# Performance work log

Hardware: AMD Instinct MI355X
Metric: run time of the kernel (lower is better)

The kernel has to match this reference:

```python
import jax, jax.numpy as jnp
import numpy as np


def gcn_conv(x, src, dst, W, b, n_nodes):
    """PyG-style GCNConv: add self-loops, symmetric deg^-1/2 normalization,
    linear transform, scatter-add aggregation to dst, then bias."""
    loop = jnp.arange(n_nodes, dtype=src.dtype)
    s = jnp.concatenate([src, loop])
    d = jnp.concatenate([dst, loop])
    deg = jax.ops.segment_sum(jnp.ones_like(d, x.dtype), d, num_segments=n_nodes)
    dinv = jax.lax.rsqrt(deg)  # deg >= 1 due to self-loops
    norm = dinv[s] * dinv[d]  # [E+N]
    h = x @ W.T  # [N, out]
    msg = h[s] * norm[:, None]  # [E+N, out]
    return jax.ops.segment_sum(msg, d, num_segments=n_nodes) + b


def setup_inputs() -> dict:
    key = jax.random.key(0)
    k = jax.random.split(key, 6)
    N, E, IN, HID, OUT = 100000, 1600000, 128, 128, 64
    x = jax.random.normal(k[0], (N, IN), dtype=jnp.float32)
    edge_index = jax.random.randint(k[1], (2, E), 0, N, dtype=jnp.int64)
    W1 = jax.random.normal(k[2], (HID, IN), dtype=jnp.float32) * 0.05
    b1 = jnp.zeros((HID,), dtype=jnp.float32)
    W2 = jax.random.normal(k[3], (OUT, HID), dtype=jnp.float32) * 0.05
    b2 = jnp.zeros((OUT,), dtype=jnp.float32)
    return {"x": x, "W1": W1, "b1": b1, "W2": W2, "b2": b2, "edge_index": edge_index}


def reference(x, W1, b1, W2, b2, edge_index):
    n_nodes = x.shape[0]
    src, dst = edge_index[0], edge_index[1]
    h = jax.nn.relu(gcn_conv(x, src, dst, W1, b1, n_nodes))
    return gcn_conv(h, src, dst, W2, b2, n_nodes)
```

## Files before the change

kernel.cpp:

```cpp
#include <hip/hip_runtime.h>
#include <hip/hip_bf16.h>


#define IN_F  128
#define HID_F 128
#define OUT_F 64

#define NPB     512
#define MAXBKT  256
#define CHUNK   4096
#define SLAB    12288
#define CAP     12288

typedef __bf16 bf16_t;
typedef __bf16 bf16x4 __attribute__((ext_vector_type(4)));
typedef __bf16 bf16x8 __attribute__((ext_vector_type(8)));
typedef float  f32x2  __attribute__((ext_vector_type(2)));
typedef float  f32x4  __attribute__((ext_vector_type(4)));
typedef unsigned u32x2 __attribute__((ext_vector_type(2)));
typedef unsigned u32x4 __attribute__((ext_vector_type(4)));

__global__ __launch_bounds__(256) void k_part(const int* __restrict__ src,
                                              const int* __restrict__ dst, int E,
                                              int* __restrict__ bcur,
                                              unsigned* __restrict__ part, int NBKT) {
    __shared__ int cnt[MAXBKT];
    __shared__ int base[MAXBKT];
    for (int i = threadIdx.x; i < NBKT; i += 256) cnt[i] = 0;
    __syncthreads();
    int cbase = blockIdx.x * CHUNK;
    int cend = min(cbase + CHUNK, E);
    for (int e = cbase + (int)threadIdx.x; e < cend; e += 256)
        atomicAdd(&cnt[dst[e] >> 9], 1);
    __syncthreads();
    int off = (int)((blockIdx.x * 73u) % (unsigned)NBKT);
    for (int j = threadIdx.x; j < NBKT; j += 256) {
        int i = j + off; if (i >= NBKT) i -= NBKT;
        int c = cnt[i];
        base[i] = c ? (i * SLAB + atomicAdd(&bcur[i * 16], c)) : 0;
        cnt[i] = 0;
    }
    __syncthreads();
    for (int e = cbase + (int)threadIdx.x; e < cend; e += 256) {
        int d = dst[e];
        int b = d >> 9;
        int lp = atomicAdd(&cnt[b], 1);
        part[base[b] + lp] = (unsigned)src[e] | ((unsigned)(d & 511) << 17);
    }
}

__global__ __launch_bounds__(512) void k_bucket(const unsigned* __restrict__ part,
                                                const int* __restrict__ bcur,
                                                int2* __restrict__ off2,
                                                int* __restrict__ col,
                                                float* __restrict__ dinv, int N) {
    __shared__ int lcnt[NPB];
    __shared__ int lexc[NPB];
    __shared__ int lcur[NPB];
    __shared__ int psum[NPB];
    __shared__ int stage[CAP];
    int b = blockIdx.x;
    int t = threadIdx.x;
    int node0 = b * NPB;
    int e0s = b * SLAB;
    int cnt = bcur[b * 16];
    lcnt[t] = 0;
    __syncthreads();
    for (int i = t; i < cnt; i += 512)
        atomicAdd(&lcnt[part[e0s + i] >> 17], 1);
    __syncthreads();
    int pc = (lcnt[t] + 7) & ~7;
    psum[t] = pc;
    __syncthreads();
    for (int ofs = 1; ofs < NPB; ofs <<= 1) {
        int add = (t >= ofs) ? psum[t - ofs] : 0;
        __syncthreads();
        psum[t] += add;
        __syncthreads();
    }
    int run = psum[t] - pc;
    lexc[t] = run;
    lcur[t] = run;
    int node = node0 + t;
    if (node < N) {
        off2[node] = make_int2(e0s + run, e0s + run + pc);
        dinv[node] = rsqrtf((float)lcnt[t] + 1.0f);
    }
    __syncthreads();
    for (int i = t; i < cnt; i += 512) {
        unsigned p = part[e0s + i];
        int dl = p >> 17;
        int sv = (int)(p & 0x1FFFF);
        int lp = atomicAdd(&lcur[dl], 1);
        if (lp < CAP) stage[lp] = sv;
        else col[e0s + lp] = sv;
    }
    __syncthreads();
    {
        int en = lexc[t] + pc;
        for (int i = lcur[t]; i < en; i++) {
            if (i < CAP) stage[i] = N; else col[e0s + i] = N;
        }
    }
    __syncthreads();
    int tot = psum[NPB - 1];
    for (int i = t; i < tot && i < CAP; i += 512) col[e0s + i] = stage[i];
}

template <int NCOL, typename TIN>
__global__ __launch_bounds__(256) void k_gemm_mfma(const TIN* __restrict__ X,
                                                   const float* __restrict__ W,
                                                   const float* __restrict__ scale,
                                                   bf16_t* __restrict__ H, int N) {
    constexpr int CT = NCOL / 16;
    int wv = threadIdx.x >> 6, lane = threadIdx.x & 63;
    int quad = lane >> 4, l16 = lane & 15;
    int row0 = blockIdx.x * 128 + wv * 32;
    f32x4 acc[2][CT] = {};
#pragma unroll
    for (int ks = 0; ks < 4; ks++) {
        int k0 = ks * 32 + quad * 8;
        bf16x8 a[2];
#pragma unroll
        for (int rt = 0; rt < 2; rt++) {
            int r = row0 + rt * 16 + l16;
            if (r >= N) r = N - 1;
            const TIN* p = X + (size_t)r * 128 + k0;
            if constexpr (sizeof(TIN) == 4) {
                f32x4 x0 = *(const f32x4*)p;
                f32x4 x1 = *(const f32x4*)(p + 4);
                bf16x8 tt;
                tt[0] = (bf16_t)x0[0]; tt[1] = (bf16_t)x0[1];
                tt[2] = (bf16_t)x0[2]; tt[3] = (bf16_t)x0[3];
                tt[4] = (bf16_t)x1[0]; tt[5] = (bf16_t)x1[1];
                tt[6] = (bf16_t)x1[2]; tt[7] = (bf16_t)x1[3];
                a[rt] = tt;
            } else {
                a[rt] = *(const bf16x8*)p;
            }
        }
#pragma unroll
        for (int ct = 0; ct < CT; ct++) {
            const float* wp = W + (size_t)(ct * 16 + l16) * 128 + k0;
            f32x4 w0 = *(const f32x4*)wp;
            f32x4 w1 = *(const f32x4*)(wp + 4);
            bf16x8 bfrag;
            bfrag[0] = (bf16_t)w0[0]; bfrag[1] = (bf16_t)w0[1];
            bfrag[2] = (bf16_t)w0[2]; bfrag[3] = (bf16_t)w0[3];
            bfrag[4] = (bf16_t)w1[0]; bfrag[5] = (bf16_t)w1[1];
            bfrag[6] = (bf16_t)w1[2]; bfrag[7] = (bf16_t)w1[3];
#pragma unroll
            for (int rt = 0; rt < 2; rt++)
                acc[rt][ct] = __builtin_amdgcn_mfma_f32_16x16x32_bf16(a[rt], bfrag, acc[rt][ct], 0, 0, 0);
        }
    }
#pragma unroll
    for (int rt = 0; rt < 2; rt++)
#pragma unroll
        for (int r4 = 0; r4 < 4; r4++) {
            int r = row0 + rt * 16 + quad * 4 + r4;
            if (r < N) {
                float sc = scale[r];
#pragma unroll
                for (int ct = 0; ct < CT; ct++)
                    H[(size_t)r * NCOL + ct * 16 + l16] = (bf16_t)(sc * acc[rt][ct][r4]);
            } else if (r == N) {
#pragma unroll
                for (int ct = 0; ct < CT; ct++)
                    H[(size_t)N * NCOL + ct * 16 + l16] = (bf16_t)0.f;
            }
        }
}

template <int ROWE>
__device__ __forceinline__ void gather8(const bf16_t* __restrict__ hp,
                                        const int* __restrict__ col, int e,
                                        u32x4* w) {
    int4 c0 = *(const int4*)(col + e);
    int4 c1 = *(const int4*)(col + e + 4);
    w[0] = *(const u32x4*)(hp + (unsigned)c0.x * (unsigned)ROWE);
    w[1] = *(const u32x4*)(hp + (unsigned)c0.y * (unsigned)ROWE);
    w[2] = *(const u32x4*)(hp + (unsigned)c0.z * (unsigned)ROWE);
    w[3] = *(const u32x4*)(hp + (unsigned)c0.w * (unsigned)ROWE);
    w[4] = *(const u32x4*)(hp + (unsigned)c1.x * (unsigned)ROWE);
    w[5] = *(const u32x4*)(hp + (unsigned)c1.y * (unsigned)ROWE);
    w[6] = *(const u32x4*)(hp + (unsigned)c1.z * (unsigned)ROWE);
    w[7] = *(const u32x4*)(hp + (unsigned)c1.w * (unsigned)ROWE);
}

__device__ __forceinline__ void accum8(const u32x4* w, f32x2* a2) {
#pragma unroll
    for (int u = 0; u < 8; u++)
#pragma unroll
        for (int k = 0; k < 4; k++) {
            f32x2 v;
            v.x = __uint_as_float(w[u][k] << 16);
            v.y = __uint_as_float(w[u][k] & 0xffff0000u);
            a2[k] += v;
        }
}

__global__ __launch_bounds__(256) void k_agg_gemm(const bf16_t* __restrict__ h,
                                                  const int2* __restrict__ off2,
                                                  const int* __restrict__ col,
                                                  const float* __restrict__ dinv,
                                                  const float* __restrict__ bias,
                                                  const float* __restrict__ W2,
                                                  bf16_t* __restrict__ h2, int N) {
    __shared__ float hl[16][132];
    __shared__ float dl[16];
    int lane = threadIdx.x & 63;
    int wv = threadIdx.x >> 6;
    int g = lane >> 4, fl = lane & 15;
    int node0 = blockIdx.x * 16;
    int node = node0 + wv * 4 + g;
    bool alive = node < N;
    int f = fl * 8;
    const bf16_t* hp = h + f;
    f32x2 a2[4] = {};
    float di = 0.f;
    if (alive) {
        u32x4 ws = *(const u32x4*)(hp + (unsigned)node * 128u);
        int2 oe = off2[node];
        di = dinv[node];
#pragma unroll
        for (int k = 0; k < 4; k++) {
            f32x2 v;
            v.x = __uint_as_float(ws[k] << 16);
            v.y = __uint_as_float(ws[k] & 0xffff0000u);
            a2[k] = v;
        }
        u32x4 w[8];
        for (int e = oe.x; e < oe.y; e += 8) {
            gather8<128>(hp, col, e, w);
            accum8(w, a2);
        }
    }
    f32x4 b0 = *(const f32x4*)(bias + f);
    f32x4 b1 = *(const f32x4*)(bias + f + 4);
    int lr = wv * 4 + g;
#pragma unroll
    for (int j = 0; j < 8; j++) {
        float bv = (j < 4) ? b0[j] : b1[j - 4];
        float val = a2[j >> 1][j & 1] * di + bv;
        hl[lr][f + j] = fmaxf(val, 0.f);
    }
    if (fl == 0) dl[lr] = di;
    __syncthreads();

    int quad = lane >> 4, l16 = lane & 15;
    f32x4 c4 = {0.f, 0.f, 0.f, 0.f};
#pragma unroll
    for (int ks = 0; ks < 4; ks++) {
        int k0 = ks * 32 + quad * 8;
        bf16x8 afr;
#pragma unroll
        for (int j = 0; j < 8; j++) afr[j] = (bf16_t)hl[l16][k0 + j];
        const float* wp = W2 + (size_t)(wv * 16 + l16) * 128 + k0;
        f32x4 w0 = *(const f32x4*)wp;
        f32x4 w1 = *(const f32x4*)(wp + 4);
        bf16x8 bfr;
        bfr[0] = (bf16_t)w0[0]; bfr[1] = (bf16_t)w0[1];
        bfr[2] = (bf16_t)w0[2]; bfr[3] = (bf16_t)w0[3];
        bfr[4] = (bf16_t)w1[0]; bfr[5] = (bf16_t)w1[1];
        bfr[6] = (bf16_t)w1[2]; bfr[7] = (bf16_t)w1[3];
        c4 = __builtin_amdgcn_mfma_f32_16x16x32_bf16(afr, bfr, c4, 0, 0, 0);
    }
#pragma unroll
    for (int r4 = 0; r4 < 4; r4++) {
        int rr = quad * 4 + r4;
        int gn = node0 + rr;
        if (gn < N)
            h2[(size_t)gn * 64 + wv * 16 + l16] = (bf16_t)(dl[rr] * c4[r4]);
    }
    if (blockIdx.x == 0 && threadIdx.x < 32)
        ((unsigned*)h2)[(size_t)N * 32 + threadIdx.x] = 0u;
}

template <int ROWE, int LPN, bool RELU, typename TOUT>
__global__ __launch_bounds__(256) void k_agg(const bf16_t* __restrict__ h,
                                             const int2* __restrict__ off2,
                                             const int* __restrict__ col,
                                             const float* __restrict__ dinv,
                                             const float* __restrict__ bias,
                                             TOUT* __restrict__ out, int N) {
    constexpr int NPW = 64 / LPN;
    int lane = threadIdx.x & 63;
    int wv = threadIdx.x >> 6;
    int g = lane / LPN, fl = lane % LPN;
    int node = blockIdx.x * (4 * NPW) + wv * NPW + g;
    if (node >= N) return;
    int f = fl * 8;
    const bf16_t* hp = h + f;
    u32x4 ws = *(const u32x4*)(hp + (unsigned)node * (unsigned)ROWE);
    int2 oe = off2[node];
    float di = dinv[node];
    f32x2 a2[4];
#pragma unroll
    for (int k = 0; k < 4; k++) {
        f32x2 v;
        v.x = __uint_as_float(ws[k] << 16);
        v.y = __uint_as_float(ws[k] & 0xffff0000u);
        a2[k] = v;
    }
    u32x4 w[8];
    for (int e = oe.x; e < oe.y; e += 8) {
        gather8<ROWE>(hp, col, e, w);
        accum8(w, a2);
    }
    f32x4 b0 = *(const f32x4*)(bias + f);
    f32x4 b1 = *(const f32x4*)(bias + f + 4);
    float r[8];
#pragma unroll
    for (int j = 0; j < 8; j++) {
        float bv = (j < 4) ? b0[j] : b1[j - 4];
        float val = a2[j >> 1][j & 1] * di + bv;
        if (RELU) val = fmaxf(val, 0.f);
        r[j] = val;
    }
    if constexpr (sizeof(TOUT) == 2) {
        bf16x8 v;
#pragma unroll
        for (int j = 0; j < 8; j++) v[j] = (bf16_t)r[j];
        *(bf16x8*)((bf16_t*)out + (size_t)node * ROWE + f) = v;
    } else {
        f32x4 v0 = {r[0], r[1], r[2], r[3]};
        f32x4 v1 = {r[4], r[5], r[6], r[7]};
        *(f32x4*)((float*)out + (size_t)node * ROWE + f) = v0;
        *(f32x4*)((float*)out + (size_t)node * ROWE + f + 4) = v1;
    }
}

extern "C" void kernel_launch(void* const* d_in, const int* in_sizes, int n_in,
                              void* d_out, int out_size, void* d_ws, size_t ws_size,
                              hipStream_t stream) {
    const float* x  = (const float*)d_in[0];
    const float* W1 = (const float*)d_in[1];
    const float* b1 = (const float*)d_in[2];
    const float* W2 = (const float*)d_in[3];
    const float* b2 = (const float*)d_in[4];
    const int*   ei = (const int*)d_in[5];

    int N = in_sizes[0] / IN_F;
    int E = in_sizes[5] / 2;
    const int* src = ei;
    const int* dst = ei + E;
    int NBKT = (N + NPB - 1) / NPB;
    int pchunks = (E + CHUNK - 1) / CHUNK;

    size_t woff = 0;
    auto alloc = [&](size_t bytes) {
        void* p = (char*)d_ws + woff;
        woff += (bytes + 255) & ~(size_t)255;
        return p;
    };
    int*      bcur  = (int*)alloc((size_t)NBKT * 16 * 4);
    unsigned* part  = (unsigned*)alloc((size_t)NBKT * SLAB * 4);
    int*      col   = (int*)alloc((size_t)NBKT * SLAB * 4);
    int2*     off2  = (int2*)alloc((size_t)N * 8);
    float*    dinv  = (float*)alloc((size_t)N * 4);
    bf16_t*   h1    = (bf16_t*)alloc((size_t)(N + 1) * HID_F * 2);
    bf16_t*   h2b   = (bf16_t*)alloc((size_t)(N + 1) * OUT_F * 2);
    float*    outp  = (float*)d_out;

    hipMemsetAsync(bcur, 0, (size_t)NBKT * 16 * 4, stream);
    k_part<<<pchunks, 256, 0, stream>>>(src, dst, E, bcur, part, NBKT);
    k_bucket<<<NBKT, 512, 0, stream>>>(part, bcur, off2, col, dinv, N);

    int gemm_blocks = (N + 127) / 128;

    k_gemm_mfma<HID_F, float><<<gemm_blocks, 256, 0, stream>>>(x, W1, dinv, h1, N);
    k_agg_gemm<<<(N + 15) / 16, 256, 0, stream>>>(h1, off2, col, dinv, b1, W2, h2b, N);
    k_agg<OUT_F, 8, false, float><<<(N + 31) / 32, 256, 0, stream>>>(h2b, off2, col, dinv, b2, outp, N);
}
```

Baseline: 271.6 us.

## Stage partition writes in LDS and pre-convert weights to bf16 once

k_part now runs a block-local prefix scan over the bucket counts and stages each edge in shared memory grouped by bucket. It then writes the chunk to the global partition buffer bucket-contiguously, so global stores are coalesced instead of scattered. A new k_pre kernel converts W1 and W2 to bf16 once and also zeroes bcur, replacing the memset. The GEMM kernels then load bf16 weight fragments directly instead of converting fp32 in every block. The staging adds about 24KB of LDS per k_part block and several scan barriers, and the scan assumes NBKT is at most 256.

Result: faster. 251.9 us (-7.3%).

```diff
diff --git a/kernel.cpp b/kernel.cpp
--- a/kernel.cpp
+++ b/kernel.cpp
@@ -20,32 +20,64 @@
 typedef unsigned u32x2 __attribute__((ext_vector_type(2)));
 typedef unsigned u32x4 __attribute__((ext_vector_type(4)));
 
+__global__ __launch_bounds__(256) void k_pre(const float* __restrict__ W1s,
+                                             const float* __restrict__ W2s,
+                                             bf16_t* __restrict__ Wdst,
+                                             int n1, int n2,
+                                             int* __restrict__ bcur, int nb16) {
+    int i = blockIdx.x * 256 + threadIdx.x;
+    if (i < n1) Wdst[i] = (bf16_t)W1s[i];
+    else if (i < n1 + n2) Wdst[i] = (bf16_t)W2s[i - n1];
+    if (blockIdx.x == gridDim.x - 1) {
+        for (int j = threadIdx.x; j < nb16; j += 256) bcur[j] = 0;
+    }
+}
+
 __global__ __launch_bounds__(256) void k_part(const int* __restrict__ src,
                                               const int* __restrict__ dst, int E,
                                               int* __restrict__ bcur,
                                               unsigned* __restrict__ part, int NBKT) {
     __shared__ int cnt[MAXBKT];
     __shared__ int base[MAXBKT];
-    for (int i = threadIdx.x; i < NBKT; i += 256) cnt[i] = 0;
+    __shared__ int cstart[MAXBKT];
+    __shared__ unsigned stg[CHUNK];
+    __shared__ unsigned short sbk[CHUNK];
+    int t = threadIdx.x;
+    cnt[t] = 0;
     __syncthreads();
     int cbase = blockIdx.x * CHUNK;
     int cend = min(cbase + CHUNK, E);
-    for (int e = cbase + (int)threadIdx.x; e < cend; e += 256)
+    int clen = cend - cbase;
+    for (int e = cbase + t; e < cend; e += 256)
         atomicAdd(&cnt[dst[e] >> 9], 1);
     __syncthreads();
-    int off = (int)((blockIdx.x * 73u) % (unsigned)NBKT);
-    for (int j = threadIdx.x; j < NBKT; j += 256) {
-        int i = j + off; if (i >= NBKT) i -= NBKT;
-        int c = cnt[i];
-        base[i] = c ? (i * SLAB + atomicAdd(&bcur[i * 16], c)) : 0;
-        cnt[i] = 0;
-    }
-    __syncthreads();
-    for (int e = cbase + (int)threadIdx.x; e < cend; e += 256) {
+    int c = cnt[t];
+    cstart[t] = c;
+    __syncthreads();
+    for (int ofs = 1; ofs < 256; ofs <<= 1) {
+        int add = (t >= ofs) ? cstart[t - ofs] : 0;
+        __syncthreads();
+        cstart[t] += add;
+        __syncthreads();
+    }
+    int excl = cstart[t] - c;
+    __syncthreads();
+    cstart[t] = excl;
+    base[t] = (c && t < NBKT) ? (t * SLAB + atomicAdd(&bcur[t * 16], c)) : 0;
+    cnt[t] = 0;
+    __syncthreads();
+    for (int e = cbase + t; e < cend; e += 256) {
         int d = dst[e];
         int b = d >> 9;
         int lp = atomicAdd(&cnt[b], 1);
-        part[base[b] + lp] = (unsigned)src[e] | ((unsigned)(d & 511) << 17);
+        int pos = cstart[b] + lp;
+        stg[pos] = (unsigned)src[e] | ((unsigned)(d & 511) << 17);
+        sbk[pos] = (unsigned short)b;
+    }
+    __syncthreads();
+    for (int i = t; i < clen; i += 256) {
+        int b = sbk[i];
+        part[base[b] + (i - cstart[b])] = stg[i];
     }
 }
 
@@ -109,7 +141,7 @@
 
 template <int NCOL, typename TIN>
 __global__ __launch_bounds__(256) void k_gemm_mfma(const TIN* __restrict__ X,
-                                                   const float* __restrict__ W,
+                                                   const bf16_t* __restrict__ W,
                                                    const float* __restrict__ scale,
                                                    bf16_t* __restrict__ H, int N) {
     constexpr int CT = NCOL / 16;
@@ -141,14 +173,7 @@
         }
 #pragma unroll
         for (int ct = 0; ct < CT; ct++) {
-            const float* wp = W + (size_t)(ct * 16 + l16) * 128 + k0;
-            f32x4 w0 = *(const f32x4*)wp;
-            f32x4 w1 = *(const f32x4*)(wp + 4);
-            bf16x8 bfrag;
-            bfrag[0] = (bf16_t)w0[0]; bfrag[1] = (bf16_t)w0[1];
-            bfrag[2] = (bf16_t)w0[2]; bfrag[3] = (bf16_t)w0[3];
-            bfrag[4] = (bf16_t)w1[0]; bfrag[5] = (bf16_t)w1[1];
-            bfrag[6] = (bf16_t)w1[2]; bfrag[7] = (bf16_t)w1[3];
+            bf16x8 bfrag = *(const bf16x8*)(W + (size_t)(ct * 16 + l16) * 128 + k0);
 #pragma unroll
             for (int rt = 0; rt < 2; rt++)
                 acc[rt][ct] = __builtin_amdgcn_mfma_f32_16x16x32_bf16(a[rt], bfrag, acc[rt][ct], 0, 0, 0);
@@ -205,7 +230,7 @@
                                                   const int* __restrict__ col,
                                                   const float* __restrict__ dinv,
                                                   const float* __restrict__ bias,
-                                                  const float* __restrict__ W2,
+                                                  const bf16_t* __restrict__ W2,
                                                   bf16_t* __restrict__ h2, int N) {
     __shared__ float hl[16][132];
     __shared__ float dl[16];
@@ -256,14 +281,7 @@
         bf16x8 afr;
 #pragma unroll
         for (int j = 0; j < 8; j++) afr[j] = (bf16_t)hl[l16][k0 + j];
-        const float* wp = W2 + (size_t)(wv * 16 + l16) * 128 + k0;
-        f32x4 w0 = *(const f32x4*)wp;
-        f32x4 w1 = *(const f32x4*)(wp + 4);
-        bf16x8 bfr;
-        bfr[0] = (bf16_t)w0[0]; bfr[1] = (bf16_t)w0[1];
-        bfr[2] = (bf16_t)w0[2]; bfr[3] = (bf16_t)w0[3];
-        bfr[4] = (bf16_t)w1[0]; bfr[5] = (bf16_t)w1[1];
-        bfr[6] = (bf16_t)w1[2]; bfr[7] = (bf16_t)w1[3];
+        bf16x8 bfr = *(const bf16x8*)(W2 + (size_t)(wv * 16 + l16) * 128 + k0);
         c4 = __builtin_amdgcn_mfma_f32_16x16x32_bf16(afr, bfr, c4, 0, 0, 0);
     }
 #pragma unroll
@@ -359,17 +377,22 @@
     int*      col   = (int*)alloc((size_t)NBKT * SLAB * 4);
     int2*     off2  = (int2*)alloc((size_t)N * 8);
     float*    dinv  = (float*)alloc((size_t)N * 4);
+    bf16_t*   Wb    = (bf16_t*)alloc((size_t)(HID_F * IN_F + OUT_F * HID_F) * 2);
+    bf16_t*   W1b   = Wb;
+    bf16_t*   W2b   = Wb + HID_F * IN_F;
     bf16_t*   h1    = (bf16_t*)alloc((size_t)(N + 1) * HID_F * 2);
     bf16_t*   h2b   = (bf16_t*)alloc((size_t)(N + 1) * OUT_F * 2);
     float*    outp  = (float*)d_out;
 
-    hipMemsetAsync(bcur, 0, (size_t)NBKT * 16 * 4, stream);
+    int n1 = HID_F * IN_F, n2 = OUT_F * HID_F;
+    int preblocks = (n1 + n2) / 256 + 1;
+    k_pre<<<preblocks, 256, 0, stream>>>(W1, W2, Wb, n1, n2, bcur, NBKT * 16);
     k_part<<<pchunks, 256, 0, stream>>>(src, dst, E, bcur, part, NBKT);
     k_bucket<<<NBKT, 512, 0, stream>>>(part, bcur, off2, col, dinv, N);
 
     int gemm_blocks = (N + 127) / 128;
 
-    k_gemm_mfma<HID_F, float><<<gemm_blocks, 256, 0, stream>>>(x, W1, dinv, h1, N);
-    k_agg_gemm<<<(N + 15) / 16, 256, 0, stream>>>(h1, off2, col, dinv, b1, W2, h2b, N);
+    k_gemm_mfma<HID_F, float><<<gemm_blocks, 256, 0, stream>>>(x, W1b, dinv, h1, N);
+    k_agg_gemm<<<(N + 15) / 16, 256, 0, stream>>>(h1, off2, col, dinv, b1, W2b, h2b, N);
     k_agg<OUT_F, 8, false, float><<<(N + 31) / 32, 256, 0, stream>>>(h2b, off2, col, dinv, b2, outp, N);
 }
```
